# Optimization experiments

Hardware: AMD Instinct MI355X
Metric: run time of the kernel (lower is better)

Reference implementation:

```python
import jax, jax.numpy as jnp
import numpy as np

CHS = [228, 111, 51]

def conv1x1(x, w, b):
    # x: [B,Cin,H,W], w: [Cout,Cin], b: [Cout]
    return jnp.einsum('bchw,oc->bohw', x, w) + b[None, :, None, None]

def prelu(x, a):
    return jnp.where(x >= 0, x, a * x)

def setup_inputs() -> dict:
    key = jax.random.key(0)
    ks = iter(jax.random.split(key, 32))
    B, H, W = 2, 256, 256
    inp = {}
    for i, c in enumerate(CHS):
        inp[f'x{i}'] = jax.random.normal(next(ks), (B, c, H, W), dtype=jnp.float32)
    for j in range(3):
        for i in range(3):
            if i == j:
                continue
            cin, cout = CHS[j], CHS[i]
            inp[f'w_{j}_{i}'] = jax.random.normal(next(ks), (cout, cin), dtype=jnp.float32) / np.sqrt(cin)
            inp[f'b_{j}_{i}'] = jax.random.normal(next(ks), (cout,), dtype=jnp.float32) * 0.01
    inp['prelu_a'] = jnp.full((1,), 0.25, dtype=jnp.float32)
    return inp

def reference(x0, x1, x2, w_0_1, b_0_1, w_0_2, b_0_2, w_1_0, b_1_0,
              w_1_2, b_1_2, w_2_0, b_2_0, w_2_1, b_2_1, prelu_a):
    W = {(0, 1): (w_0_1, b_0_1), (0, 2): (w_0_2, b_0_2),
         (1, 0): (w_1_0, b_1_0), (1, 2): (w_1_2, b_1_2),
         (2, 0): (w_2_0, b_2_0), (2, 1): (w_2_1, b_2_1)}
    a = prelu_a[0]
    h = [x0, x1, x2]
    for _ in range(2):  # self.iters = 2, weights shared across iterations
        h_new = []
        for i in range(3):
            binary = None
            for j in range(3):
                if i == j:
                    continue
                w, b = W[(j, i)]
                msg = conv1x1(h[j], w, b)
                binary = msg if binary is None else binary + msg
            h_new.append(jax.nn.relu(h[i] + prelu(binary, a)))
        h = h_new
    # concat along channels (as CRFVGG_prune aggregates branch outputs)
    return jnp.concatenate(h, axis=1)
```

## Files before the change

### kernel.cpp

```cpp
#include <hip/hip_runtime.h>
#include <stdint.h>

typedef __attribute__((ext_vector_type(8))) short short8;
typedef __attribute__((ext_vector_type(4))) float f32x4;
typedef __attribute__((ext_vector_type(2))) unsigned int uint2v;

#define C0 228
#define C1 111
#define C2 51
#define KP 448
#define RS 456
#define NPIX 64

__device__ __forceinline__ unsigned short f2bf(float f) {
  unsigned u = __float_as_uint(f);
  u += 0x7FFFu + ((u >> 16) & 1u);
  return (unsigned short)(u >> 16);
}
__device__ __forceinline__ float bf2f(unsigned v) {
  return __uint_as_float(v << 16);
}

__device__ __forceinline__ int out_chan(int c) {
  if (c < 228) return c;
  if (c < 256) return -1;
  if (c < 367) return 228 + (c - 256);
  if (c < 384) return -1;
  if (c < 435) return 339 + (c - 384);
  return -1;
}

__global__ void crf_prep(
    const float* __restrict__ w01, const float* __restrict__ w02,
    const float* __restrict__ w10, const float* __restrict__ w12,
    const float* __restrict__ w20, const float* __restrict__ w21,
    const float* __restrict__ b01, const float* __restrict__ b02,
    const float* __restrict__ b10, const float* __restrict__ b12,
    const float* __restrict__ b20, const float* __restrict__ b21,
    unsigned short* __restrict__ Wrow, float* __restrict__ bbig) {
  int idx = blockIdx.x * 256 + threadIdx.x;
  if (idx >= KP * KP) return;
  int m = idx / KP;
  int k = idx - m * KP;
  int bm, lm, bk, lk, Ck;
  bool mr, kr;
  if (m < 256)      { bm = 0; lm = m;       mr = lm < C0; }
  else if (m < 384) { bm = 1; lm = m - 256; mr = lm < C1; }
  else              { bm = 2; lm = m - 384; mr = lm < C2; }
  if (k < 256)      { bk = 0; lk = k;       Ck = C0; kr = lk < C0; }
  else if (k < 384) { bk = 1; lk = k - 256; Ck = C1; kr = lk < C1; }
  else              { bk = 2; lk = k - 384; Ck = C2; kr = lk < C2; }
  float v = 0.f;
  if (bm != bk && mr && kr) {
    const float* w;
    if (bk == 0)      w = (bm == 1) ? w01 : w02;
    else if (bk == 1) w = (bm == 0) ? w10 : w12;
    else              w = (bm == 0) ? w20 : w21;
    v = w[lm * Ck + lk];
  }
  Wrow[idx] = f2bf(v);
  if (idx < KP) {
    float bv = 0.f;
    int c = idx;
    if (c < 228)                  bv = b10[c] + b20[c];
    else if (c >= 256 && c < 367) bv = b01[c - 256] + b21[c - 256];
    else if (c >= 384 && c < 435) bv = b02[c - 384] + b12[c - 384];
    bbig[idx] = bv;
  }
}

__global__ __launch_bounds__(512, 4) void crf_main(
    const float* __restrict__ x0, const float* __restrict__ x1,
    const float* __restrict__ x2,
    const unsigned short* __restrict__ Wrow,
    const float* __restrict__ bbig,
    const float* __restrict__ pa,
    float* __restrict__ out) {
  __shared__ unsigned short hL[NPIX][RS];
  const int lane = threadIdx.x & 63;
  const int wave = threadIdx.x >> 6;
  const int tile = blockIdx.x;
  const int b = tile >> 10;
  const int pp0 = (tile & 1023) << 6;
  const float apar = pa[0];
  const bool has3 = (wave < 4);

  #pragma unroll
  for (int g = 0; g < 7; ++g) {
    const int c0 = (wave + g * 8) * 8;
    short8 pk;
    #pragma unroll
    for (int cc = 0; cc < 8; ++cc) {
      const int c = c0 + cc;
      float v = 0.f;
      if (c < 228)
        v = __builtin_nontemporal_load(
            x0 + (((size_t)(b * C0 + c)) << 16) + pp0 + lane);
      else if (c >= 256 && c < 367)
        v = __builtin_nontemporal_load(
            x1 + (((size_t)(b * C1 + (c - 256))) << 16) + pp0 + lane);
      else if (c >= 384 && c < 435)
        v = __builtin_nontemporal_load(
            x2 + (((size_t)(b * C2 + (c - 384))) << 16) + pp0 + lane);
      pk[cc] = (short)f2bf(v);
    }
    *reinterpret_cast<short8*>(&hL[lane][c0]) = pk;
  }
  __syncthreads();

  const int l15 = lane & 15;
  const int lq = lane >> 4;

  #pragma unroll
  for (int it = 0; it < 2; ++it) {
    f32x4 acc[4][4];
    #pragma unroll
    for (int t = 0; t < 4; ++t)
      #pragma unroll
      for (int n = 0; n < 4; ++n)
        acc[t][n] = (f32x4){0.f, 0.f, 0.f, 0.f};

    #pragma unroll
    for (int ks = 0; ks < 14; ++ks) {
      const int kb = (ks < 8) ? 0 : ((ks < 12) ? 1 : 2);
      const int kcol = ks * 32 + (lq << 3);
      short8 bq[4];
      #pragma unroll
      for (int n = 0; n < 4; ++n)
        bq[n] = *reinterpret_cast<const short8*>(&hL[n * 16 + l15][kcol]);
      #pragma unroll
      for (int t = 0; t < 4; ++t) {
        const int bm = (t < 2) ? 0 : ((t < 3) ? 1 : 2);
        if (bm == kb) continue;
        if (t == 3 && !has3) continue;
        const int mt = wave + 8 * t;
        const short8 aq = *reinterpret_cast<const short8*>(
            Wrow + (mt * 16 + l15) * KP + kcol);
        #pragma unroll
        for (int n = 0; n < 4; ++n)
          acc[t][n] =
              __builtin_amdgcn_mfma_f32_16x16x32_bf16(aq, bq[n], acc[t][n], 0, 0, 0);
      }
    }
    __syncthreads();

    if (it == 0) {
      #pragma unroll
      for (int t = 0; t < 4; ++t) {
        if (t == 3 && !has3) continue;
        const int cb = (wave + 8 * t) * 16 + (lq << 2);
        const f32x4 bias = *reinterpret_cast<const f32x4*>(bbig + cb);
        #pragma unroll
        for (int n = 0; n < 4; ++n) {
          const int p = n * 16 + l15;
          uint2v ho = *reinterpret_cast<const uint2v*>(&hL[p][cb]);
          const float hof[4] = {bf2f(ho[0] & 0xFFFFu), bf2f(ho[0] >> 16),
                                bf2f(ho[1] & 0xFFFFu), bf2f(ho[1] >> 16)};
          unsigned short nb[4];
          #pragma unroll
          for (int r = 0; r < 4; ++r) {
            float v = acc[t][n][r] + bias[r];
            float pr = (v >= 0.f) ? v : apar * v;
            nb[r] = f2bf(fmaxf(hof[r] + pr, 0.f));
          }
          uint2v pw;
          pw[0] = (unsigned)nb[0] | ((unsigned)nb[1] << 16);
          pw[1] = (unsigned)nb[2] | ((unsigned)nb[3] << 16);
          *reinterpret_cast<uint2v*>(&hL[p][cb]) = pw;
        }
      }
      __syncthreads();
    } else {
      #pragma unroll
      for (int t = 0; t < 4; ++t) {
        if (t == 3 && !has3) continue;
        const int cb = (wave + 8 * t) * 16 + (lq << 2);
        const f32x4 bias = *reinterpret_cast<const f32x4*>(bbig + cb);
        #pragma unroll
        for (int n = 0; n < 4; ++n) {
          const int p = n * 16 + l15;
          uint2v ho = *reinterpret_cast<const uint2v*>(&hL[p][cb]);
          const float hof[4] = {bf2f(ho[0] & 0xFFFFu), bf2f(ho[0] >> 16),
                                bf2f(ho[1] & 0xFFFFu), bf2f(ho[1] >> 16)};
          #pragma unroll
          for (int r = 0; r < 4; ++r) {
            const int c = cb + r;
            const int o = out_chan(c);
            float v = acc[t][n][r] + bias[r];
            float pr = (v >= 0.f) ? v : apar * v;
            float hn = fmaxf(hof[r] + pr, 0.f);
            if (o >= 0)
              __builtin_nontemporal_store(
                  hn, out + (((size_t)(b * 390 + o)) << 16) + pp0 + p);
          }
        }
      }
    }
  }
}

extern "C" void kernel_launch(void* const* d_in, const int* in_sizes, int n_in,
                              void* d_out, int out_size, void* d_ws, size_t ws_size,
                              hipStream_t stream) {
  const float* x0  = (const float*)d_in[0];
  const float* x1  = (const float*)d_in[1];
  const float* x2  = (const float*)d_in[2];
  const float* w01 = (const float*)d_in[3];
  const float* b01 = (const float*)d_in[4];
  const float* w02 = (const float*)d_in[5];
  const float* b02 = (const float*)d_in[6];
  const float* w10 = (const float*)d_in[7];
  const float* b10 = (const float*)d_in[8];
  const float* w12 = (const float*)d_in[9];
  const float* b12 = (const float*)d_in[10];
  const float* w20 = (const float*)d_in[11];
  const float* b20 = (const float*)d_in[12];
  const float* w21 = (const float*)d_in[13];
  const float* b21 = (const float*)d_in[14];
  const float* pa  = (const float*)d_in[15];

  unsigned short* Wrow = (unsigned short*)d_ws;
  float* bbig = (float*)((char*)d_ws + (size_t)KP * KP * 2);

  crf_prep<<<dim3((KP * KP + 255) / 256), dim3(256), 0, stream>>>(
      w01, w02, w10, w12, w20, w21, b01, b02, b10, b12, b20, b21, Wrow, bbig);
  crf_main<<<dim3(2048), dim3(512), 0, stream>>>(x0, x1, x2, Wrow, bbig, pa,
                                                 (float*)d_out);
}
```

Measured before the change: 201.8 us.

## Make blocks persistent with register-resident weights and double-buffered input prefetch

Each block now handles 8 consecutive 64-pixel tiles (256 blocks instead of 2048) and keeps its 28 bf16 weight fragments in registers, loaded once from a fragment-ordered layout that the prep kernel writes. Work is rebalanced so each wave runs exactly 28 MFMA k-steps with no skipped blocks. The next tile's input is loaded from global memory in two halves, overlapped with the two GEMM iterations, and written into a second LDS buffer. The aim is to remove repeated global weight reads and hide input-load latency, at the cost of more registers, lower occupancy (launch bounds 2) and only 256 blocks, which may not fill the GPU.

```diff
diff --git a/kernel.cpp b/kernel.cpp
--- a/kernel.cpp
+++ b/kernel.cpp
@@ -11,6 +11,18 @@
 #define KP 448
 #define RS 456
 #define NPIX 64
+#define BUFE (NPIX * RS)
+#define DYN_LDS (2 * BUFE * 2)
+
+constexpr int A_KS[28] = {0,1,2,3,4,5,6,7,8,8,8,9,9,9,10,10,10,11,11,11,12,12,12,12,13,13,13,13};
+constexpr int A_T [28] = {3,3,3,3,3,3,3,3,0,1,2,0,1,2, 0, 1, 2, 0, 1, 2, 0, 1, 2, 3, 0, 1, 2, 3};
+constexpr int B_KS[28] = {0,0,1,1,2,2,3,3,4,4,5,5,6,6,7,7,8,8,9,9,10,10,11,11,12,12,13,13};
+constexpr int B_T [28] = {1,2,1,2,1,2,1,2,1,2,1,2,1,2,1,2,0,2,0,2, 0, 2, 0, 2, 0, 1, 0, 1};
+
+__host__ __device__ constexpr int tile_id(int w, int t) {
+  return (w < 4) ? ((t < 3) ? (3 * w + t) : (16 + w))
+                 : ((t == 0) ? (8 + w) : (t == 1) ? (16 + w) : (20 + w));
+}
 
 __device__ __forceinline__ unsigned short f2bf(float f) {
   unsigned u = __float_as_uint(f);
@@ -20,7 +32,6 @@
 __device__ __forceinline__ float bf2f(unsigned v) {
   return __uint_as_float(v << 16);
 }
-
 __device__ __forceinline__ int out_chan(int c) {
   if (c < 228) return c;
   if (c < 256) return -1;
@@ -30,6 +41,13 @@
   return -1;
 }
 
+__device__ __forceinline__ void barrier_lgkm() {
+  __builtin_amdgcn_sched_barrier(0);
+  asm volatile("s_waitcnt lgkmcnt(0)" ::: "memory");
+  __builtin_amdgcn_s_barrier();
+  __builtin_amdgcn_sched_barrier(0);
+}
+
 __global__ void crf_prep(
     const float* __restrict__ w01, const float* __restrict__ w02,
     const float* __restrict__ w10, const float* __restrict__ w12,
@@ -37,11 +55,28 @@
     const float* __restrict__ b01, const float* __restrict__ b02,
     const float* __restrict__ b10, const float* __restrict__ b12,
     const float* __restrict__ b20, const float* __restrict__ b21,
-    unsigned short* __restrict__ Wrow, float* __restrict__ bbig) {
+    unsigned short* __restrict__ Wfrag, float* __restrict__ bbig) {
   int idx = blockIdx.x * 256 + threadIdx.x;
-  if (idx >= KP * KP) return;
-  int m = idx / KP;
-  int k = idx - m * KP;
+  if (idx < KP) {
+    float bv = 0.f;
+    int c = idx;
+    if (c < 228)                  bv = b10[c] + b20[c];
+    else if (c >= 256 && c < 367) bv = b01[c - 256] + b21[c - 256];
+    else if (c >= 384 && c < 435) bv = b02[c - 384] + b12[c - 384];
+    bbig[idx] = bv;
+  }
+  if (idx >= 224 * 512) return;
+  const int ch = idx >> 9;
+  const int e  = idx & 511;
+  const int w  = ch / 28;
+  const int s  = ch - w * 28;
+  const int ks = (w < 4) ? A_KS[s] : B_KS[s];
+  const int tl = (w < 4) ? A_T[s]  : B_T[s];
+  const int tile = tile_id(w, tl);
+  const int lane = e >> 3, el = e & 7;
+  const int m = tile * 16 + (lane & 15);
+  const int k = ks * 32 + (lane >> 4) * 8 + el;
+
   int bm, lm, bk, lk, Ck;
   bool mr, kr;
   if (m < 256)      { bm = 0; lm = m;       mr = lm < C0; }
@@ -52,150 +87,191 @@
   else              { bk = 2; lk = k - 384; Ck = C2; kr = lk < C2; }
   float v = 0.f;
   if (bm != bk && mr && kr) {
-    const float* w;
-    if (bk == 0)      w = (bm == 1) ? w01 : w02;
-    else if (bk == 1) w = (bm == 0) ? w10 : w12;
-    else              w = (bm == 0) ? w20 : w21;
-    v = w[lm * Ck + lk];
-  }
-  Wrow[idx] = f2bf(v);
-  if (idx < KP) {
-    float bv = 0.f;
-    int c = idx;
-    if (c < 228)                  bv = b10[c] + b20[c];
-    else if (c >= 256 && c < 367) bv = b01[c - 256] + b21[c - 256];
-    else if (c >= 384 && c < 435) bv = b02[c - 384] + b12[c - 384];
-    bbig[idx] = bv;
-  }
-}
-
-__global__ __launch_bounds__(512, 4) void crf_main(
+    const float* wp;
+    if (bk == 0)      wp = (bm == 1) ? w01 : w02;
+    else if (bk == 1) wp = (bm == 0) ? w10 : w12;
+    else              wp = (bm == 0) ? w20 : w21;
+    v = wp[lm * Ck + lk];
+  }
+  Wfrag[idx] = f2bf(v);
+}
+
+template <int NG, int G0>
+__device__ __forceinline__ void stage_load(int wave, int lane, int b, int pp,
+    const float* __restrict__ x0, const float* __restrict__ x1,
+    const float* __restrict__ x2, float (*dst)[8]) {
+  #pragma unroll
+  for (int gg = 0; gg < NG; ++gg) {
+    const int cg = (wave + 8 * (G0 + gg)) * 8;
+    #pragma unroll
+    for (int cc = 0; cc < 8; ++cc) {
+      const int c = cg + cc;
+      float v = 0.f;
+      if (c < 228)
+        v = __builtin_nontemporal_load(x0 + (((size_t)(b * C0 + c)) << 16) + pp + lane);
+      else if (c >= 256 && c < 367)
+        v = __builtin_nontemporal_load(x1 + (((size_t)(b * C1 + (c - 256))) << 16) + pp + lane);
+      else if (c >= 384 && c < 435)
+        v = __builtin_nontemporal_load(x2 + (((size_t)(b * C2 + (c - 384))) << 16) + pp + lane);
+      dst[gg][cc] = v;
+    }
+  }
+}
+
+template <int NG, int G0>
+__device__ __forceinline__ void stage_write(int wave, int lane, float (*src)[8],
+                                            unsigned short* __restrict__ nxt) {
+  #pragma unroll
+  for (int gg = 0; gg < NG; ++gg) {
+    const int cg = (wave + 8 * (G0 + gg)) * 8;
+    short8 pk;
+    #pragma unroll
+    for (int cc = 0; cc < 8; ++cc) pk[cc] = (short)f2bf(src[gg][cc]);
+    *reinterpret_cast<short8*>(nxt + lane * RS + cg) = pk;
+  }
+}
+
+template <int CLS>
+__device__ __forceinline__ void kloop(const unsigned short* __restrict__ cur,
+                                      const short8 (&wreg)[28], f32x4 (&acc)[4][4],
+                                      int l15, int lq) {
+  short8 bq[4];
+  #pragma unroll
+  for (int s = 0; s < 28; ++s) {
+    const int ks = CLS ? B_KS[s] : A_KS[s];
+    const int t  = CLS ? B_T[s]  : A_T[s];
+    const bool newks = (s == 0) || (ks != (CLS ? B_KS[s - 1] : A_KS[s - 1]));
+    if (newks) {
+      const int kcol = ks * 32 + (lq << 3);
+      #pragma unroll
+      for (int n = 0; n < 4; ++n)
+        bq[n] = *reinterpret_cast<const short8*>(cur + (n * 16 + l15) * RS + kcol);
+    }
+    #pragma unroll
+    for (int n = 0; n < 4; ++n)
+      acc[t][n] = __builtin_amdgcn_mfma_f32_16x16x32_bf16(wreg[s], bq[n], acc[t][n], 0, 0, 0);
+  }
+}
+
+__global__ __launch_bounds__(512, 2) void crf_main(
     const float* __restrict__ x0, const float* __restrict__ x1,
     const float* __restrict__ x2,
-    const unsigned short* __restrict__ Wrow,
+    const unsigned short* __restrict__ Wfrag,
     const float* __restrict__ bbig,
     const float* __restrict__ pa,
     float* __restrict__ out) {
-  __shared__ unsigned short hL[NPIX][RS];
+  extern __shared__ unsigned short hbuf[];
   const int lane = threadIdx.x & 63;
   const int wave = threadIdx.x >> 6;
-  const int tile = blockIdx.x;
-  const int b = tile >> 10;
-  const int pp0 = (tile & 1023) << 6;
-  const float apar = pa[0];
-  const bool has3 = (wave < 4);
-
-  #pragma unroll
-  for (int g = 0; g < 7; ++g) {
-    const int c0 = (wave + g * 8) * 8;
-    short8 pk;
-    #pragma unroll
-    for (int cc = 0; cc < 8; ++cc) {
-      const int c = c0 + cc;
-      float v = 0.f;
-      if (c < 228)
-        v = __builtin_nontemporal_load(
-            x0 + (((size_t)(b * C0 + c)) << 16) + pp0 + lane);
-      else if (c >= 256 && c < 367)
-        v = __builtin_nontemporal_load(
-            x1 + (((size_t)(b * C1 + (c - 256))) << 16) + pp0 + lane);
-      else if (c >= 384 && c < 435)
-        v = __builtin_nontemporal_load(
-            x2 + (((size_t)(b * C2 + (c - 384))) << 16) + pp0 + lane);
-      pk[cc] = (short)f2bf(v);
-    }
-    *reinterpret_cast<short8*>(&hL[lane][c0]) = pk;
-  }
-  __syncthreads();
-
   const int l15 = lane & 15;
   const int lq = lane >> 4;
-
-  #pragma unroll
-  for (int it = 0; it < 2; ++it) {
+  const float apar = pa[0];
+
+  short8 wreg[28];
+  {
+    const unsigned short* wp = Wfrag + (((size_t)wave * 28) << 9) + lane * 8;
+    #pragma unroll
+    for (int s = 0; s < 28; ++s)
+      wreg[s] = *reinterpret_cast<const short8*>(wp + (s << 9));
+  }
+
+  const int T0 = blockIdx.x * 8;
+  const int b = (T0 >= 1024) ? 1 : 0;
+  const int ppbase = (T0 & 1023) << 6;
+
+  {
+    float sA[4][8], sB[3][8];
+    stage_load<4, 0>(wave, lane, b, ppbase, x0, x1, x2, sA);
+    stage_load<3, 4>(wave, lane, b, ppbase, x0, x1, x2, sB);
+    stage_write<4, 0>(wave, lane, sA, hbuf);
+    stage_write<3, 4>(wave, lane, sB, hbuf);
+  }
+  barrier_lgkm();
+
+  for (int i = 0; i < 8; ++i) {
+    unsigned short* cur = hbuf + (i & 1) * BUFE;
+    unsigned short* nxt = hbuf + ((i + 1) & 1) * BUFE;
+    const int pp0 = ppbase + (i << 6);
+    const int pp1 = pp0 + 64;
+    const bool more = (i < 7);
+
+    float s0[4][8];
+    if (more) stage_load<4, 0>(wave, lane, b, pp1, x0, x1, x2, s0);
+
     f32x4 acc[4][4];
     #pragma unroll
     for (int t = 0; t < 4; ++t)
       #pragma unroll
-      for (int n = 0; n < 4; ++n)
-        acc[t][n] = (f32x4){0.f, 0.f, 0.f, 0.f};
-
-    #pragma unroll
-    for (int ks = 0; ks < 14; ++ks) {
-      const int kb = (ks < 8) ? 0 : ((ks < 12) ? 1 : 2);
-      const int kcol = ks * 32 + (lq << 3);
-      short8 bq[4];
-      #pragma unroll
-      for (int n = 0; n < 4; ++n)
-        bq[n] = *reinterpret_cast<const short8*>(&hL[n * 16 + l15][kcol]);
-      #pragma unroll
-      for (int t = 0; t < 4; ++t) {
-        const int bm = (t < 2) ? 0 : ((t < 3) ? 1 : 2);
-        if (bm == kb) continue;
-        if (t == 3 && !has3) continue;
-        const int mt = wave + 8 * t;
-        const short8 aq = *reinterpret_cast<const short8*>(
-            Wrow + (mt * 16 + l15) * KP + kcol);
+      for (int n = 0; n < 4; ++n) acc[t][n] = (f32x4){0.f, 0.f, 0.f, 0.f};
+    if (wave < 4) kloop<0>(cur, wreg, acc, l15, lq);
+    else          kloop<1>(cur, wreg, acc, l15, lq);
+
+    if (more) stage_write<4, 0>(wave, lane, s0, nxt);
+    barrier_lgkm();
+
+    #pragma unroll
+    for (int t = 0; t < 4; ++t) {
+      if (t == 3 && wave >= 4) continue;
+      const int cb = tile_id(wave, t) * 16 + (lq << 2);
+      const f32x4 bias = *reinterpret_cast<const f32x4*>(bbig + cb);
+      #pragma unroll
+      for (int n = 0; n < 4; ++n) {
+        const int p = n * 16 + l15;
+        uint2v ho = *reinterpret_cast<const uint2v*>(cur + p * RS + cb);
+        const float hof[4] = {bf2f(ho[0] & 0xFFFFu), bf2f(ho[0] >> 16),
+                              bf2f(ho[1] & 0xFFFFu), bf2f(ho[1] >> 16)};
+        unsigned short nb[4];
         #pragma unroll
-        for (int n = 0; n < 4; ++n)
-          acc[t][n] =
-              __builtin_amdgcn_mfma_f32_16x16x32_bf16(aq, bq[n], acc[t][n], 0, 0, 0);
+        for (int r = 0; r < 4; ++r) {
+          float v = acc[t][n][r] + bias[r];
+          float pr = (v >= 0.f) ? v : apar * v;
+          nb[r] = f2bf(fmaxf(hof[r] + pr, 0.f));
+        }
+        uint2v pw;
+        pw[0] = (unsigned)nb[0] | ((unsigned)nb[1] << 16);
+        pw[1] = (unsigned)nb[2] | ((unsigned)nb[3] << 16);
+        *reinterpret_cast<uint2v*>(cur + p * RS + cb) = pw;
       }
     }
-    __syncthreads();
-
-    if (it == 0) {
-      #pragma unroll
-      for (int t = 0; t < 4; ++t) {
-        if (t == 3 && !has3) continue;
-        const int cb = (wave + 8 * t) * 16 + (lq << 2);
-        const f32x4 bias = *reinterpret_cast<const f32x4*>(bbig + cb);
+
+    float s1[3][8];
+    if (more) stage_load<3, 4>(wave, lane, b, pp1, x0, x1, x2, s1);
+    barrier_lgkm();
+
+    #pragma unroll
+    for (int t = 0; t < 4; ++t)
+      #pragma unroll
+      for (int n = 0; n < 4; ++n) acc[t][n] = (f32x4){0.f, 0.f, 0.f, 0.f};
+    if (wave < 4) kloop<0>(cur, wreg, acc, l15, lq);
+    else          kloop<1>(cur, wreg, acc, l15, lq);
+
+    #pragma unroll
+    for (int t = 0; t < 4; ++t) {
+      if (t == 3 && wave >= 4) continue;
+      const int cb = tile_id(wave, t) * 16 + (lq << 2);
+      const f32x4 bias = *reinterpret_cast<const f32x4*>(bbig + cb);
+      #pragma unroll
+      for (int n = 0; n < 4; ++n) {
+        const int p = n * 16 + l15;
+        uint2v ho = *reinterpret_cast<const uint2v*>(cur + p * RS + cb);
+        const float hof[4] = {bf2f(ho[0] & 0xFFFFu), bf2f(ho[0] >> 16),
+                              bf2f(ho[1] & 0xFFFFu), bf2f(ho[1] >> 16)};
         #pragma unroll
-        for (int n = 0; n < 4; ++n) {
-          const int p = n * 16 + l15;
-          uint2v ho = *reinterpret_cast<const uint2v*>(&hL[p][cb]);
-          const float hof[4] = {bf2f(ho[0] & 0xFFFFu), bf2f(ho[0] >> 16),
-                                bf2f(ho[1] & 0xFFFFu), bf2f(ho[1] >> 16)};
-          unsigned short nb[4];
-          #pragma unroll
-          for (int r = 0; r < 4; ++r) {
-            float v = acc[t][n][r] + bias[r];
-            float pr = (v >= 0.f) ? v : apar * v;
-            nb[r] = f2bf(fmaxf(hof[r] + pr, 0.f));
-          }
-          uint2v pw;
-          pw[0] = (unsigned)nb[0] | ((unsigned)nb[1] << 16);
-          pw[1] = (unsigned)nb[2] | ((unsigned)nb[3] << 16);
-          *reinterpret_cast<uint2v*>(&hL[p][cb]) = pw;
-        }
-      }
-      __syncthreads();
-    } else {
-      #pragma unroll
-      for (int t = 0; t < 4; ++t) {
-        if (t == 3 && !has3) continue;
-        const int cb = (wave + 8 * t) * 16 + (lq << 2);
-        const f32x4 bias = *reinterpret_cast<const f32x4*>(bbig + cb);
-        #pragma unroll
-        for (int n = 0; n < 4; ++n) {
-          const int p = n * 16 + l15;
-          uint2v ho = *reinterpret_cast<const uint2v*>(&hL[p][cb]);
-          const float hof[4] = {bf2f(ho[0] & 0xFFFFu), bf2f(ho[0] >> 16),
-                                bf2f(ho[1] & 0xFFFFu), bf2f(ho[1] >> 16)};
-          #pragma unroll
-          for (int r = 0; r < 4; ++r) {
-            const int c = cb + r;
-            const int o = out_chan(c);
-            float v = acc[t][n][r] + bias[r];
-            float pr = (v >= 0.f) ? v : apar * v;
-            float hn = fmaxf(hof[r] + pr, 0.f);
-            if (o >= 0)
-              __builtin_nontemporal_store(
-                  hn, out + (((size_t)(b * 390 + o)) << 16) + pp0 + p);
-          }
+        for (int r = 0; r < 4; ++r) {
+          const int c = cb + r;
+          const int o = out_chan(c);
+          float v = acc[t][n][r] + bias[r];
+          float pr = (v >= 0.f) ? v : apar * v;
+          float hn = fmaxf(hof[r] + pr, 0.f);
+          if (o >= 0)
+            __builtin_nontemporal_store(
+                hn, out + (((size_t)(b * 390 + o)) << 16) + pp0 + p);
         }
       }
     }
+
+    if (more) stage_write<3, 4>(wave, lane, s1, nxt);
+    barrier_lgkm();
   }
 }
 
@@ -219,11 +295,14 @@
   const float* b21 = (const float*)d_in[14];
   const float* pa  = (const float*)d_in[15];
 
-  unsigned short* Wrow = (unsigned short*)d_ws;
-  float* bbig = (float*)((char*)d_ws + (size_t)KP * KP * 2);
-
-  crf_prep<<<dim3((KP * KP + 255) / 256), dim3(256), 0, stream>>>(
-      w01, w02, w10, w12, w20, w21, b01, b02, b10, b12, b20, b21, Wrow, bbig);
-  crf_main<<<dim3(2048), dim3(512), 0, stream>>>(x0, x1, x2, Wrow, bbig, pa,
-                                                 (float*)d_out);
-}
+  unsigned short* Wfrag = (unsigned short*)d_ws;
+  float* bbig = (float*)((char*)d_ws + 224 * 512 * 2);
+
+  hipFuncSetAttribute((const void*)crf_main,
+                      hipFuncAttributeMaxDynamicSharedMemorySize, DYN_LDS);
+
+  crf_prep<<<dim3(448), dim3(256), 0, stream>>>(
+      w01, w02, w10, w12, w20, w21, b01, b02, b10, b12, b20, b21, Wfrag, bbig);
+  crf_main<<<dim3(256), dim3(512), DYN_LDS, stream>>>(x0, x1, x2, Wfrag, bbig, pa,
+                                                      (float*)d_out);
+}
```

After: 492.6 us. +144.2%, slower.

## Warp-specialize crf_main with producer waves double-buffering input tiles in LDS

Applied to the files above, without the earlier changes.

Makes the main kernel persistent-style: each block handles 8 consecutive 64-pixel tiles using 8 consumer waves for MFMA and epilogue work and 4 producer waves that load and convert the next tile into a second LDS buffer. The aim is to hide global load latency behind the GEMM of the current tile instead of serialising the load phase per block. It doubles LDS per block, reduces the grid to 256 blocks, and adds explicit barriers between phases, so occupancy and load balance across CUs change.

```diff
diff --git a/kernel.cpp b/kernel.cpp
--- a/kernel.cpp
+++ b/kernel.cpp
@@ -11,6 +11,8 @@
 #define KP 448
 #define RS 456
 #define NPIX 64
+#define BUFE (NPIX * RS)
+#define DYN_LDS (2 * BUFE * 2)
 
 __device__ __forceinline__ unsigned short f2bf(float f) {
   unsigned u = __float_as_uint(f);
@@ -20,7 +22,6 @@
 __device__ __forceinline__ float bf2f(unsigned v) {
   return __uint_as_float(v << 16);
 }
-
 __device__ __forceinline__ int out_chan(int c) {
   if (c < 228) return c;
   if (c < 256) return -1;
@@ -28,6 +29,13 @@
   if (c < 384) return -1;
   if (c < 435) return 339 + (c - 384);
   return -1;
+}
+
+__device__ __forceinline__ void barrier_lgkm() {
+  __builtin_amdgcn_sched_barrier(0);
+  asm volatile("s_waitcnt lgkmcnt(0)" ::: "memory");
+  __builtin_amdgcn_s_barrier();
+  __builtin_amdgcn_sched_barrier(0);
 }
 
 __global__ void crf_prep(
@@ -69,82 +77,114 @@
   }
 }
 
-__global__ __launch_bounds__(512, 4) void crf_main(
+template <int NG, int G0>
+__device__ __forceinline__ void produce(int pw, int lane, int b, int pp,
+    const float* __restrict__ x0, const float* __restrict__ x1,
+    const float* __restrict__ x2, unsigned short* __restrict__ nxt) {
+  float v[NG][8];
+  #pragma unroll
+  for (int g = 0; g < NG; ++g) {
+    const int c0 = (pw * 14 + G0 + g) * 8;
+    #pragma unroll
+    for (int cc = 0; cc < 8; ++cc) {
+      const int c = c0 + cc;
+      float t = 0.f;
+      if (c < 228)
+        t = __builtin_nontemporal_load(x0 + (((size_t)(b * C0 + c)) << 16) + pp + lane);
+      else if (c >= 256 && c < 367)
+        t = __builtin_nontemporal_load(x1 + (((size_t)(b * C1 + (c - 256))) << 16) + pp + lane);
+      else if (c >= 384 && c < 435)
+        t = __builtin_nontemporal_load(x2 + (((size_t)(b * C2 + (c - 384))) << 16) + pp + lane);
+      v[g][cc] = t;
+    }
+  }
+  #pragma unroll
+  for (int g = 0; g < NG; ++g) {
+    const int c0 = (pw * 14 + G0 + g) * 8;
+    short8 pk;
+    #pragma unroll
+    for (int cc = 0; cc < 8; ++cc) pk[cc] = (short)f2bf(v[g][cc]);
+    *reinterpret_cast<short8*>(nxt + lane * RS + c0) = pk;
+  }
+}
+
+__device__ __forceinline__ void kloop(const unsigned short* __restrict__ cur,
+                                      const unsigned short* __restrict__ Wrow,
+                                      f32x4 (&acc)[4][4], int wave, bool has3,
+                                      int l15, int lq) {
+  #pragma unroll
+  for (int ks = 0; ks < 14; ++ks) {
+    const int kb = (ks < 8) ? 0 : ((ks < 12) ? 1 : 2);
+    const int kcol = ks * 32 + (lq << 3);
+    short8 bq[4];
+    #pragma unroll
+    for (int n = 0; n < 4; ++n)
+      bq[n] = *reinterpret_cast<const short8*>(cur + (n * 16 + l15) * RS + kcol);
+    #pragma unroll
+    for (int t = 0; t < 4; ++t) {
+      const int bm = (t < 2) ? 0 : ((t < 3) ? 1 : 2);
+      if (bm == kb) continue;
+      if (t == 3 && !has3) continue;
+      const int mt = wave + 8 * t;
+      const short8 aq = *reinterpret_cast<const short8*>(
+          Wrow + (mt * 16 + l15) * KP + kcol);
+      #pragma unroll
+      for (int n = 0; n < 4; ++n)
+        acc[t][n] =
+            __builtin_amdgcn_mfma_f32_16x16x32_bf16(aq, bq[n], acc[t][n], 0, 0, 0);
+    }
+  }
+}
+
+__global__ __launch_bounds__(768, 3) void crf_main(
     const float* __restrict__ x0, const float* __restrict__ x1,
     const float* __restrict__ x2,
     const unsigned short* __restrict__ Wrow,
     const float* __restrict__ bbig,
     const float* __restrict__ pa,
     float* __restrict__ out) {
-  __shared__ unsigned short hL[NPIX][RS];
+  extern __shared__ unsigned short hbuf[];
   const int lane = threadIdx.x & 63;
   const int wave = threadIdx.x >> 6;
-  const int tile = blockIdx.x;
-  const int b = tile >> 10;
-  const int pp0 = (tile & 1023) << 6;
+  const bool is_cons = (wave < 8);
+  const int pw = wave - 8;
+  const int l15 = lane & 15;
+  const int lq = lane >> 4;
   const float apar = pa[0];
   const bool has3 = (wave < 4);
 
-  #pragma unroll
-  for (int g = 0; g < 7; ++g) {
-    const int c0 = (wave + g * 8) * 8;
-    short8 pk;
-    #pragma unroll
-    for (int cc = 0; cc < 8; ++cc) {
-      const int c = c0 + cc;
-      float v = 0.f;
-      if (c < 228)
-        v = __builtin_nontemporal_load(
-            x0 + (((size_t)(b * C0 + c)) << 16) + pp0 + lane);
-      else if (c >= 256 && c < 367)
-        v = __builtin_nontemporal_load(
-            x1 + (((size_t)(b * C1 + (c - 256))) << 16) + pp0 + lane);
-      else if (c >= 384 && c < 435)
-        v = __builtin_nontemporal_load(
-            x2 + (((size_t)(b * C2 + (c - 384))) << 16) + pp0 + lane);
-      pk[cc] = (short)f2bf(v);
-    }
-    *reinterpret_cast<short8*>(&hL[lane][c0]) = pk;
-  }
-  __syncthreads();
-
-  const int l15 = lane & 15;
-  const int lq = lane >> 4;
-
-  #pragma unroll
-  for (int it = 0; it < 2; ++it) {
+  const int T0 = blockIdx.x * 8;
+  const int b = (T0 >= 1024) ? 1 : 0;
+  const int ppbase = (T0 & 1023) << 6;
+
+  if (!is_cons) {
+    produce<5, 0>(pw, lane, b, ppbase, x0, x1, x2, hbuf);
+    produce<5, 5>(pw, lane, b, ppbase, x0, x1, x2, hbuf);
+    produce<4, 10>(pw, lane, b, ppbase, x0, x1, x2, hbuf);
+  }
+  barrier_lgkm();
+
+  for (int i = 0; i < 8; ++i) {
+    unsigned short* cur = hbuf + (i & 1) * BUFE;
+    unsigned short* nxt = hbuf + ((i + 1) & 1) * BUFE;
+    const int pp0 = ppbase + (i << 6);
+    const int pp1 = pp0 + 64;
+    const bool more = (i < 7);
+
     f32x4 acc[4][4];
-    #pragma unroll
-    for (int t = 0; t < 4; ++t)
-      #pragma unroll
-      for (int n = 0; n < 4; ++n)
-        acc[t][n] = (f32x4){0.f, 0.f, 0.f, 0.f};
-
-    #pragma unroll
-    for (int ks = 0; ks < 14; ++ks) {
-      const int kb = (ks < 8) ? 0 : ((ks < 12) ? 1 : 2);
-      const int kcol = ks * 32 + (lq << 3);
-      short8 bq[4];
-      #pragma unroll
-      for (int n = 0; n < 4; ++n)
-        bq[n] = *reinterpret_cast<const short8*>(&hL[n * 16 + l15][kcol]);
-      #pragma unroll
-      for (int t = 0; t < 4; ++t) {
-        const int bm = (t < 2) ? 0 : ((t < 3) ? 1 : 2);
-        if (bm == kb) continue;
-        if (t == 3 && !has3) continue;
-        const int mt = wave + 8 * t;
-        const short8 aq = *reinterpret_cast<const short8*>(
-            Wrow + (mt * 16 + l15) * KP + kcol);
-        #pragma unroll
-        for (int n = 0; n < 4; ++n)
-          acc[t][n] =
-              __builtin_amdgcn_mfma_f32_16x16x32_bf16(aq, bq[n], acc[t][n], 0, 0, 0);
-      }
-    }
-    __syncthreads();
-
-    if (it == 0) {
+
+    if (is_cons) {
+      #pragma unroll
+      for (int t = 0; t < 4; ++t)
+        #pragma unroll
+        for (int n = 0; n < 4; ++n) acc[t][n] = (f32x4){0.f, 0.f, 0.f, 0.f};
+      kloop(cur, Wrow, acc, wave, has3, l15, lq);
+    } else if (more) {
+      produce<5, 0>(pw, lane, b, pp1, x0, x1, x2, nxt);
+    }
+    barrier_lgkm();
+
+    if (is_cons) {
       #pragma unroll
       for (int t = 0; t < 4; ++t) {
         if (t == 3 && !has3) continue;
@@ -153,7 +193,7 @@
         #pragma unroll
         for (int n = 0; n < 4; ++n) {
           const int p = n * 16 + l15;
-          uint2v ho = *reinterpret_cast<const uint2v*>(&hL[p][cb]);
+          uint2v ho = *reinterpret_cast<const uint2v*>(cur + p * RS + cb);
           const float hof[4] = {bf2f(ho[0] & 0xFFFFu), bf2f(ho[0] >> 16),
                                 bf2f(ho[1] & 0xFFFFu), bf2f(ho[1] >> 16)};
           unsigned short nb[4];
@@ -163,14 +203,23 @@
             float pr = (v >= 0.f) ? v : apar * v;
             nb[r] = f2bf(fmaxf(hof[r] + pr, 0.f));
           }
-          uint2v pw;
-          pw[0] = (unsigned)nb[0] | ((unsigned)nb[1] << 16);
-          pw[1] = (unsigned)nb[2] | ((unsigned)nb[3] << 16);
-          *reinterpret_cast<uint2v*>(&hL[p][cb]) = pw;
+          uint2v pwv;
+          pwv[0] = (unsigned)nb[0] | ((unsigned)nb[1] << 16);
+          pwv[1] = (unsigned)nb[2] | ((unsigned)nb[3] << 16);
+          *reinterpret_cast<uint2v*>(cur + p * RS + cb) = pwv;
         }
       }
-      __syncthreads();
-    } else {
+    } else if (more) {
+      produce<5, 5>(pw, lane, b, pp1, x0, x1, x2, nxt);
+    }
+    barrier_lgkm();
+
+    if (is_cons) {
+      #pragma unroll
+      for (int t = 0; t < 4; ++t)
+        #pragma unroll
+        for (int n = 0; n < 4; ++n) acc[t][n] = (f32x4){0.f, 0.f, 0.f, 0.f};
+      kloop(cur, Wrow, acc, wave, has3, l15, lq);
       #pragma unroll
       for (int t = 0; t < 4; ++t) {
         if (t == 3 && !has3) continue;
@@ -179,7 +228,7 @@
         #pragma unroll
         for (int n = 0; n < 4; ++n) {
           const int p = n * 16 + l15;
-          uint2v ho = *reinterpret_cast<const uint2v*>(&hL[p][cb]);
+          uint2v ho = *reinterpret_cast<const uint2v*>(cur + p * RS + cb);
           const float hof[4] = {bf2f(ho[0] & 0xFFFFu), bf2f(ho[0] >> 16),
                                 bf2f(ho[1] & 0xFFFFu), bf2f(ho[1] >> 16)};
           #pragma unroll
@@ -195,7 +244,10 @@
           }
         }
       }
-    }
+    } else if (more) {
+      produce<4, 10>(pw, lane, b, pp1, x0, x1, x2, nxt);
+    }
+    barrier_lgkm();
   }
 }
 
@@ -222,8 +274,11 @@
   unsigned short* Wrow = (unsigned short*)d_ws;
   float* bbig = (float*)((char*)d_ws + (size_t)KP * KP * 2);
 
+  hipFuncSetAttribute((const void*)crf_main,
+                      hipFuncAttributeMaxDynamicSharedMemorySize, DYN_LDS);
+
   crf_prep<<<dim3((KP * KP + 255) / 256), dim3(256), 0, stream>>>(
       w01, w02, w10, w12, w20, w21, b01, b02, b10, b12, b20, b21, Wrow, bbig);
-  crf_main<<<dim3(2048), dim3(512), 0, stream>>>(x0, x1, x2, Wrow, bbig, pa,
-                                                 (float*)d_out);
-}
+  crf_main<<<dim3(256), dim3(768), DYN_LDS, stream>>>(x0, x1, x2, Wrow, bbig, pa,
+                                                      (float*)d_out);
+}
```

Measured after the change: 724.3 us. +259.0%, slower.

## Preload balanced weight fragments into registers with per-wave MFMA schedule

Applied to the files above, without the earlier changes.

Weights are repacked in the prep kernel into per-wave, per-step MFMA fragment order, and each wave loads its 28 weight fragments into registers once instead of re-reading global weights every k-step in both iterations. Output tiles are reassigned so every wave does exactly 28 MFMA groups, evening out work that was previously uneven because waves 4-7 had fewer tiles. The LDS row stride is changed and launch bounds are lowered to 2 blocks per SM to make room for the larger register footprint, trading occupancy for fewer global loads.

```diff
diff --git a/kernel.cpp b/kernel.cpp
--- a/kernel.cpp
+++ b/kernel.cpp
@@ -9,8 +9,18 @@
 #define C1 111
 #define C2 51
 #define KP 448
-#define RS 456
+#define RS 458
 #define NPIX 64
+
+constexpr int A_KS[28] = {0,1,2,3,4,5,6,7,8,8,8,9,9,9,10,10,10,11,11,11,12,12,12,12,13,13,13,13};
+constexpr int A_T [28] = {3,3,3,3,3,3,3,3,0,1,2,0,1,2, 0, 1, 2, 0, 1, 2, 0, 1, 2, 3, 0, 1, 2, 3};
+constexpr int B_KS[28] = {0,0,1,1,2,2,3,3,4,4,5,5,6,6,7,7,8,8,9,9,10,10,11,11,12,12,13,13};
+constexpr int B_T [28] = {1,2,1,2,1,2,1,2,1,2,1,2,1,2,1,2,0,2,0,2, 0, 2, 0, 2, 0, 1, 0, 1};
+
+__host__ __device__ constexpr int tile_id(int w, int t) {
+  return (w < 4) ? ((t < 3) ? (3 * w + t) : (16 + w))
+                 : ((t == 0) ? (8 + w) : (t == 1) ? (16 + w) : (20 + w));
+}
 
 __device__ __forceinline__ unsigned short f2bf(float f) {
   unsigned u = __float_as_uint(f);
@@ -20,7 +30,6 @@
 __device__ __forceinline__ float bf2f(unsigned v) {
   return __uint_as_float(v << 16);
 }
-
 __device__ __forceinline__ int out_chan(int c) {
   if (c < 228) return c;
   if (c < 256) return -1;
@@ -37,11 +46,28 @@
     const float* __restrict__ b01, const float* __restrict__ b02,
     const float* __restrict__ b10, const float* __restrict__ b12,
     const float* __restrict__ b20, const float* __restrict__ b21,
-    unsigned short* __restrict__ Wrow, float* __restrict__ bbig) {
+    unsigned short* __restrict__ Wfrag, float* __restrict__ bbig) {
   int idx = blockIdx.x * 256 + threadIdx.x;
-  if (idx >= KP * KP) return;
-  int m = idx / KP;
-  int k = idx - m * KP;
+  if (idx < KP) {
+    float bv = 0.f;
+    int c = idx;
+    if (c < 228)                  bv = b10[c] + b20[c];
+    else if (c >= 256 && c < 367) bv = b01[c - 256] + b21[c - 256];
+    else if (c >= 384 && c < 435) bv = b02[c - 384] + b12[c - 384];
+    bbig[idx] = bv;
+  }
+  if (idx >= 224 * 512) return;
+  const int ch = idx >> 9;
+  const int e  = idx & 511;
+  const int w  = ch / 28;
+  const int s  = ch - w * 28;
+  const int ks = (w < 4) ? A_KS[s] : B_KS[s];
+  const int tl = (w < 4) ? A_T[s]  : B_T[s];
+  const int tile = tile_id(w, tl);
+  const int lane = e >> 3, el = e & 7;
+  const int m = tile * 16 + (lane & 15);
+  const int k = ks * 32 + (lane >> 4) * 8 + el;
+
   int bm, lm, bk, lk, Ck;
   bool mr, kr;
   if (m < 256)      { bm = 0; lm = m;       mr = lm < C0; }
@@ -52,38 +78,62 @@
   else              { bk = 2; lk = k - 384; Ck = C2; kr = lk < C2; }
   float v = 0.f;
   if (bm != bk && mr && kr) {
-    const float* w;
-    if (bk == 0)      w = (bm == 1) ? w01 : w02;
-    else if (bk == 1) w = (bm == 0) ? w10 : w12;
-    else              w = (bm == 0) ? w20 : w21;
-    v = w[lm * Ck + lk];
-  }
-  Wrow[idx] = f2bf(v);
-  if (idx < KP) {
-    float bv = 0.f;
-    int c = idx;
-    if (c < 228)                  bv = b10[c] + b20[c];
-    else if (c >= 256 && c < 367) bv = b01[c - 256] + b21[c - 256];
-    else if (c >= 384 && c < 435) bv = b02[c - 384] + b12[c - 384];
-    bbig[idx] = bv;
-  }
-}
-
-__global__ __launch_bounds__(512, 4) void crf_main(
+    const float* wp;
+    if (bk == 0)      wp = (bm == 1) ? w01 : w02;
+    else if (bk == 1) wp = (bm == 0) ? w10 : w12;
+    else              wp = (bm == 0) ? w20 : w21;
+    v = wp[lm * Ck + lk];
+  }
+  Wfrag[idx] = f2bf(v);
+}
+
+template <int CLS>
+__device__ __forceinline__ void kloop(const unsigned short (*cur)[RS],
+                                      const short8 (&wreg)[28], f32x4 (&acc)[4][4],
+                                      int l15, int lq) {
+  short8 bq[4];
+  #pragma unroll
+  for (int s = 0; s < 28; ++s) {
+    const int ks = CLS ? B_KS[s] : A_KS[s];
+    const int t  = CLS ? B_T[s]  : A_T[s];
+    const bool newks = (s == 0) || (ks != (CLS ? B_KS[s - 1] : A_KS[s - 1]));
+    if (newks) {
+      const int kcol = ks * 32 + (lq << 3);
+      #pragma unroll
+      for (int n = 0; n < 4; ++n)
+        bq[n] = *reinterpret_cast<const short8*>(&cur[n * 16 + l15][kcol]);
+    }
+    #pragma unroll
+    for (int n = 0; n < 4; ++n)
+      acc[t][n] =
+          __builtin_amdgcn_mfma_f32_16x16x32_bf16(wreg[s], bq[n], acc[t][n], 0, 0, 0);
+  }
+}
+
+__global__ __launch_bounds__(512, 2) void crf_main(
     const float* __restrict__ x0, const float* __restrict__ x1,
     const float* __restrict__ x2,
-    const unsigned short* __restrict__ Wrow,
+    const unsigned short* __restrict__ Wfrag,
     const float* __restrict__ bbig,
     const float* __restrict__ pa,
     float* __restrict__ out) {
   __shared__ unsigned short hL[NPIX][RS];
   const int lane = threadIdx.x & 63;
   const int wave = threadIdx.x >> 6;
+  const int l15 = lane & 15;
+  const int lq = lane >> 4;
+  const float apar = pa[0];
   const int tile = blockIdx.x;
   const int b = tile >> 10;
   const int pp0 = (tile & 1023) << 6;
-  const float apar = pa[0];
-  const bool has3 = (wave < 4);
+
+  short8 wreg[28];
+  {
+    const unsigned short* wp = Wfrag + (((size_t)wave * 28) << 9) + (lane << 3);
+    #pragma unroll
+    for (int s = 0; s < 28; ++s)
+      wreg[s] = *reinterpret_cast<const short8*>(wp + (s << 9));
+  }
 
   #pragma unroll
   for (int g = 0; g < 7; ++g) {
@@ -94,61 +144,34 @@
       const int c = c0 + cc;
       float v = 0.f;
       if (c < 228)
-        v = __builtin_nontemporal_load(
-            x0 + (((size_t)(b * C0 + c)) << 16) + pp0 + lane);
+        v = __builtin_nontemporal_load(x0 + (((size_t)(b * C0 + c)) << 16) + pp0 + lane);
       else if (c >= 256 && c < 367)
-        v = __builtin_nontemporal_load(
-            x1 + (((size_t)(b * C1 + (c - 256))) << 16) + pp0 + lane);
+        v = __builtin_nontemporal_load(x1 + (((size_t)(b * C1 + (c - 256))) << 16) + pp0 + lane);
       else if (c >= 384 && c < 435)
-        v = __builtin_nontemporal_load(
-            x2 + (((size_t)(b * C2 + (c - 384))) << 16) + pp0 + lane);
+        v = __builtin_nontemporal_load(x2 + (((size_t)(b * C2 + (c - 384))) << 16) + pp0 + lane);
       pk[cc] = (short)f2bf(v);
     }
     *reinterpret_cast<short8*>(&hL[lane][c0]) = pk;
   }
   __syncthreads();
 
-  const int l15 = lane & 15;
-  const int lq = lane >> 4;
-
   #pragma unroll
   for (int it = 0; it < 2; ++it) {
     f32x4 acc[4][4];
     #pragma unroll
     for (int t = 0; t < 4; ++t)
       #pragma unroll
-      for (int n = 0; n < 4; ++n)
-        acc[t][n] = (f32x4){0.f, 0.f, 0.f, 0.f};
-
-    #pragma unroll
-    for (int ks = 0; ks < 14; ++ks) {
-      const int kb = (ks < 8) ? 0 : ((ks < 12) ? 1 : 2);
-      const int kcol = ks * 32 + (lq << 3);
-      short8 bq[4];
-      #pragma unroll
-      for (int n = 0; n < 4; ++n)
-        bq[n] = *reinterpret_cast<const short8*>(&hL[n * 16 + l15][kcol]);
+      for (int n = 0; n < 4; ++n) acc[t][n] = (f32x4){0.f, 0.f, 0.f, 0.f};
+
+    if (wave < 4) kloop<0>(hL, wreg, acc, l15, lq);
+    else          kloop<1>(hL, wreg, acc, l15, lq);
+    __syncthreads();
+
+    if (it == 0) {
       #pragma unroll
       for (int t = 0; t < 4; ++t) {
-        const int bm = (t < 2) ? 0 : ((t < 3) ? 1 : 2);
-        if (bm == kb) continue;
-        if (t == 3 && !has3) continue;
-        const int mt = wave + 8 * t;
-        const short8 aq = *reinterpret_cast<const short8*>(
-            Wrow + (mt * 16 + l15) * KP + kcol);
-        #pragma unroll
-        for (int n = 0; n < 4; ++n)
-          acc[t][n] =
-              __builtin_amdgcn_mfma_f32_16x16x32_bf16(aq, bq[n], acc[t][n], 0, 0, 0);
-      }
-    }
-    __syncthreads();
-
-    if (it == 0) {
-      #pragma unroll
-      for (int t = 0; t < 4; ++t) {
-        if (t == 3 && !has3) continue;
-        const int cb = (wave + 8 * t) * 16 + (lq << 2);
+        if (t == 3 && wave >= 4) continue;
+        const int cb = tile_id(wave, t) * 16 + (lq << 2);
         const f32x4 bias = *reinterpret_cast<const f32x4*>(bbig + cb);
         #pragma unroll
         for (int n = 0; n < 4; ++n) {
@@ -173,8 +196,8 @@
     } else {
       #pragma unroll
       for (int t = 0; t < 4; ++t) {
-        if (t == 3 && !has3) continue;
-        const int cb = (wave + 8 * t) * 16 + (lq << 2);
+        if (t == 3 && wave >= 4) continue;
+        const int cb = tile_id(wave, t) * 16 + (lq << 2);
         const f32x4 bias = *reinterpret_cast<const f32x4*>(bbig + cb);
         #pragma unroll
         for (int n = 0; n < 4; ++n) {
@@ -219,11 +242,11 @@
   const float* b21 = (const float*)d_in[14];
   const float* pa  = (const float*)d_in[15];
 
-  unsigned short* Wrow = (unsigned short*)d_ws;
-  float* bbig = (float*)((char*)d_ws + (size_t)KP * KP * 2);
-
-  crf_prep<<<dim3((KP * KP + 255) / 256), dim3(256), 0, stream>>>(
-      w01, w02, w10, w12, w20, w21, b01, b02, b10, b12, b20, b21, Wrow, bbig);
-  crf_main<<<dim3(2048), dim3(512), 0, stream>>>(x0, x1, x2, Wrow, bbig, pa,
+  unsigned short* Wfrag = (unsigned short*)d_ws;
+  float* bbig = (float*)((char*)d_ws + 224 * 512 * 2);
+
+  crf_prep<<<dim3(448), dim3(256), 0, stream>>>(
+      w01, w02, w10, w12, w20, w21, b01, b02, b10, b12, b20, b21, Wfrag, bbig);
+  crf_main<<<dim3(2048), dim3(512), 0, stream>>>(x0, x1, x2, Wfrag, bbig, pa,
                                                  (float*)d_out);
 }
```

New measurement: 358.3 us. 1.78x slower.
